# Optimization experiments

Measured on AMD Instinct MI355X. Metric: run time of the kernel, lower is better.

The kernel has to match this reference:

```python
import jax, jax.numpy as jnp
import numpy as np

D_MODEL = 1024
RANK = 256
INIT_ALPHA = 0.5


def setup_inputs() -> dict:
    key = jax.random.key(0)
    ks = jax.random.split(key, 12)
    D, R = D_MODEL, RANK
    s = 0.02
    return {
        "x": jax.random.normal(ks[0], (4, 2048, D), dtype=jnp.float32),
        "Wq": jax.random.normal(ks[1], (D, D), dtype=jnp.float32) * s,
        "Wk": jax.random.normal(ks[2], (D, D), dtype=jnp.float32) * s,
        "Wo": jax.random.normal(ks[3], (D, D), dtype=jnp.float32) * s,
        "U_b": jax.random.normal(ks[4], (D, R), dtype=jnp.float32) * s,
        "V_b": jax.random.normal(ks[5], (D, R), dtype=jnp.float32) * s,
        "W_b": jax.random.normal(ks[6], (D, R), dtype=jnp.float32) * s,
        "bias_b": jnp.zeros((D,), dtype=jnp.float32),
        "U_t": jax.random.normal(ks[7], (D, R), dtype=jnp.float32) * s,
        "V_t": jax.random.normal(ks[8], (D, R), dtype=jnp.float32) * s,
        "W_t": jax.random.normal(ks[9], (D, R), dtype=jnp.float32) * s,
        "X_t": jax.random.normal(ks[10], (D, R), dtype=jnp.float32) * s,
        "bias_t": jnp.zeros((D,), dtype=jnp.float32),
        "alpha": jnp.asarray(INIT_ALPHA, dtype=jnp.float32),
    }


def reference(x, Wq, Wk, Wo, U_b, V_b, W_b, bias_b, U_t, V_t, W_t, X_t, bias_t, alpha):
    # Math identical to the original O(T^2 D) materialization (attention_mask=None path),
    # reduced to causal cumulative sums: sum_{j<=i} (q_i * k_j) = q_i * cumsum_j(k_j).
    B, T, D = x.shape
    Q = x @ Wq.T                      # [B,T,D] (nn.Linear: x @ W^T)
    K = x @ Wk.T
    counts = jnp.arange(1, T + 1, dtype=x.dtype)[None, :, None]  # [1,T,1]
    Z = jnp.cumsum(x, axis=1) / counts  # causal cumulative mean [B,T,D]

    # Bilinear: sum_{j<=i} ((Q_i V_b) * (K_j W_b)) U_b^T + bias_b (per j)
    a_b = Q @ V_b                     # [B,T,R]
    c_b = jnp.cumsum(K @ W_b, axis=1) # [B,T,R] causal sum over j
    bil = (a_b * c_b) @ U_b.T         # [B,T,D]

    # Trilinear: sum_{j<=i} ((Q_i V_t) * (K_j W_t) * (Z_i X_t)) U_t^T + bias_t
    a_t = Q @ V_t
    c_t = jnp.cumsum(K @ W_t, axis=1)
    z_t = Z @ X_t
    tri = (a_t * z_t * c_t) @ U_t.T   # [B,T,D]

    # Per-i division by n_valid = i+1; the per-(i,j) biases average back to themselves.
    out = (bil + alpha * tri) / counts + (bias_b + alpha * bias_t)
    return out @ Wo.T                 # W_O (dropout=0 -> identity)
```

## Files before the change

kernel.cpp:

```cpp
#include <hip/hip_runtime.h>

#define D_MODEL 1024
#define RANK    256
#define NBATCH  4
#define TSEQ    2048
#define MROWS   (NBATCH * TSEQ)
#define NCAT    1280
#define NE      512

#define OFF_WQT   0u
#define OFF_WKT   524288u
#define OFF_WOB   1048576u
#define OFF_VCT   1572864u
#define OFF_WCT   1835008u
#define OFF_UCT   2097152u
#define OFF_B2    2359296u
#define OFF_PB    2360320u
#define OFF_GB    3015680u
#define OFF_Y     3277824u
#define OFF_SCR   13763584u
#define OFF_XB    13861888u
#define OFF_EB    OFF_XB

typedef __attribute__((ext_vector_type(8))) short bf16x8;
typedef __attribute__((ext_vector_type(4))) float f32x4;

__device__ __forceinline__ unsigned short f2bf(float f) {
  union { float f; unsigned u; } v; v.f = f;
  return (unsigned short)((v.u + 0x7fff + ((v.u >> 16) & 1)) >> 16);
}

__device__ __forceinline__ void gload16(const void* g, void* l) {
  __builtin_amdgcn_global_load_lds(
      (const __attribute__((address_space(1))) unsigned*)g,
      (__attribute__((address_space(3))) unsigned*)l, 16, 0, 0);
}

template <int EPI, int OBF>
__device__ __forceinline__ void mfma_tile(
    const short* __restrict__ A, const short* __restrict__ B, void* __restrict__ Cv,
    int K, int ldA, int ldB, int ldC, int m0, int n0,
    const float* __restrict__ bias, short* As, short* Bs) {
  const int tid = threadIdx.x;
  const int l = tid & 63;
  const int wv = tid >> 6;
  const int wm = (wv >> 1) * 64, wn = (wv & 1) * 64;

  const int sr = tid >> 2;
  const int sc = (tid & 3) * 8;
  const short* gA = A + (size_t)(m0 + sr) * ldA + sc;
  const short* gB = B + (size_t)(n0 + sr) * ldB + sc;
  short* lA = As + sr * 32 + sc;
  short* lB = Bs + sr * 32 + sc;

  const int arow = wm + (l & 15);
  const int brow = wn + (l & 15);
  const int kc = (l >> 4) * 8;

  f32x4 acc[4][4] = {};

  for (int k0 = 0; k0 < K; k0 += 32) {
    gload16(gA, lA);
    gload16(gA + (size_t)64 * ldA, lA + 64 * 32);
    gload16(gB, lB);
    gload16(gB + (size_t)64 * ldB, lB + 64 * 32);
    gA += 32; gB += 32;
    __syncthreads();

    bf16x8 af[4], bfr[4];
#pragma unroll
    for (int m = 0; m < 4; ++m) af[m] = *(const bf16x8*)&As[(arow + m * 16) * 32 + kc];
#pragma unroll
    for (int n = 0; n < 4; ++n) bfr[n] = *(const bf16x8*)&Bs[(brow + n * 16) * 32 + kc];

#pragma unroll
    for (int m = 0; m < 4; ++m)
#pragma unroll
      for (int n = 0; n < 4; ++n)
        acc[m][n] = __builtin_amdgcn_mfma_f32_16x16x32_bf16(af[m], bfr[n], acc[m][n], 0, 0, 0);
    __syncthreads();
  }

  const int cc = wn + (l & 15);
  const int crb = wm + (l >> 4) * 4;
#pragma unroll
  for (int m = 0; m < 4; ++m) {
#pragma unroll
    for (int j = 0; j < 4; ++j) {
      const int gm = m0 + crb + m * 16 + j;
      float inv = 1.0f;
      if (EPI) inv = 1.0f / (float)((gm & (TSEQ - 1)) + 1);
#pragma unroll
      for (int n = 0; n < 4; ++n) {
        const int gn = n0 + cc + n * 16;
        float v = acc[m][n][j];
        if (EPI) v = v * inv + bias[gn];
        if (OBF) ((short*)Cv)[(size_t)gm * ldC + gn] = (short)f2bf(v);
        else     ((float*)Cv)[(size_t)gm * ldC + gn] = v;
      }
    }
  }
}

template <int EPI>
__global__ __launch_bounds__(256) void mfma_nt(
    const short* __restrict__ A, const short* __restrict__ B,
    float* __restrict__ C, int K, int ldA, int ldB, int ldC,
    const float* __restrict__ bias) {
  __shared__ short As[128 * 32];
  __shared__ short Bs[128 * 32];
  mfma_tile<EPI, 0>(A, B, C, K, ldA, ldB, ldC,
                    blockIdx.y * 128, blockIdx.x * 128, bias, As, Bs);
}

__global__ __launch_bounds__(256) void prep_mfma(
    const short* __restrict__ VCT, const short* __restrict__ WQT,
    const short* __restrict__ WCT, const short* __restrict__ WKT,
    const short* __restrict__ WOB, const short* __restrict__ UCT,
    short* __restrict__ Pb, short* __restrict__ Gb) {
  __shared__ short As[128 * 32];
  __shared__ short Bs[128 * 32];
  const int g = blockIdx.x >> 5, t = blockIdx.x & 31;
  if (g == 0)
    mfma_tile<0, 1>(VCT, WQT, Pb, 1024, 1024, 1024, 1024,
                    (t >> 3) * 128, (t & 7) * 128, nullptr, As, Bs);
  else if (g == 1)
    mfma_tile<0, 1>(WCT, WKT, Pb + (size_t)512 * 1024, 1024, 1024, 1024, 1024,
                    (t >> 3) * 128, (t & 7) * 128, nullptr, As, Bs);
  else
    mfma_tile<0, 1>(WOB, UCT, Gb, 1024, 1024, 1024, 512,
                    (t >> 2) * 128, (t & 3) * 128, nullptr, As, Bs);
}

__global__ __launch_bounds__(256) void trans_kernel(
    const float* __restrict__ Vb, const float* __restrict__ Vt,
    const float* __restrict__ Wb, const float* __restrict__ Wt,
    const float* __restrict__ Ub, const float* __restrict__ Ut,
    const float* __restrict__ Xt, const float* __restrict__ Wq,
    const float* __restrict__ Wk,
    short* __restrict__ VCT, short* __restrict__ WCT, short* __restrict__ UCT,
    short* __restrict__ PbXt, short* __restrict__ WQT, short* __restrict__ WKT) {
  const int bid = blockIdx.x;
  const int tid = threadIdx.x;
  const float* src; short* O; int r0, d0, c0, ldS;
  if (bid < 384) {
    const int z = bid >> 7, t = bid & 127;
    r0 = (t >> 4) * 64; d0 = (t & 15) * 64; ldS = 256;
    const float* S0 = z == 0 ? Vb : z == 1 ? Wb : Ub;
    const float* S1 = z == 0 ? Vt : z == 1 ? Wt : Ut;
    O = z == 0 ? VCT : z == 1 ? WCT : UCT;
    src = (r0 < 256) ? S0 : S1; c0 = r0 & 255;
  } else if (bid < 448) {
    const int t = bid - 384;
    r0 = (t >> 4) * 64; d0 = (t & 15) * 64; ldS = 256;
    src = Xt; c0 = r0; O = PbXt;
  } else {
    const int t = bid - 448;
    const int w = t >> 8, tt = t & 255;
    r0 = (tt >> 4) * 64; d0 = (tt & 15) * 64; ldS = 1024;
    src = w ? Wk : Wq; O = w ? WKT : WQT; c0 = r0;
  }
  __shared__ float Ts[64][65];
  const int lr = tid >> 4;
  const int lc = (tid & 15) * 4;
#pragma unroll
  for (int p = 0; p < 4; ++p) {
    const int row = lr + p * 16;
    const float4 v = *(const float4*)&src[(size_t)(d0 + row) * ldS + c0 + lc];
    Ts[row][lc + 0] = v.x; Ts[row][lc + 1] = v.y;
    Ts[row][lc + 2] = v.z; Ts[row][lc + 3] = v.w;
  }
  __syncthreads();
#pragma unroll
  for (int p = 0; p < 4; ++p) {
    const int ri = lr + p * 16;
    ushort4 o;
    o.x = f2bf(Ts[lc + 0][ri]); o.y = f2bf(Ts[lc + 1][ri]);
    o.z = f2bf(Ts[lc + 2][ri]); o.w = f2bf(Ts[lc + 3][ri]);
    *(ushort4*)&((unsigned short*)O)[(size_t)(r0 + ri) * 1024 + d0 + lc] = o;
  }
}

__global__ void f2b_kernel(const float* __restrict__ in, short* __restrict__ out, int n) {
  const int i = (blockIdx.x * blockDim.x + threadIdx.x) * 4;
  if (i >= n) return;
  const float4 v = *(const float4*)&in[i];
  ushort4 o;
  o.x = f2bf(v.x); o.y = f2bf(v.y); o.z = f2bf(v.z); o.w = f2bf(v.w);
  *(ushort4*)&out[i] = o;
}

__global__ void bias_proj(const float* __restrict__ Wo, const float* __restrict__ bias_b,
                          const float* __restrict__ bias_t, const float* __restrict__ alpha_p,
                          float* __restrict__ b2) {
  const float al = *alpha_p;
  const int d = blockIdx.x;
  const int t = threadIdx.x;
  float s = 0.f;
  for (int e = t; e < 1024; e += 256)
    s += Wo[(size_t)d * 1024 + e] * (bias_b[e] + al * bias_t[e]);
  __shared__ float red[256];
  red[t] = s; __syncthreads();
  for (int off = 128; off > 0; off >>= 1) {
    if (t < off) red[t] += red[t + off];
    __syncthreads();
  }
  if (t == 0) b2[d] = red[0];
}

#define CUMCOLS 768
__global__ void cumsum_s1(const float* __restrict__ Y, float* __restrict__ scr) {
  const int lane = threadIdx.x;
  const int cg = blockIdx.x, seg = blockIdx.y, b = blockIdx.z;
  const int col = 512 + cg * 64 + lane;
  size_t base = (size_t)(b * TSEQ + seg * 64) * NCAT + col;
  float s = 0.f;
  for (int t = 0; t < 64; ++t) s += Y[base + (size_t)t * NCAT];
  scr[(size_t)(b * 32 + seg) * CUMCOLS + cg * 64 + lane] = s;
}
__global__ void cumsum_s2(float* __restrict__ scr) {
  const int lane = threadIdx.x;
  const int cg = blockIdx.x, b = blockIdx.z;
  const int c = cg * 64 + lane;
  float run = 0.f;
  for (int seg = 0; seg < 32; ++seg) {
    const size_t idx = (size_t)(b * 32 + seg) * CUMCOLS + c;
    const float v = scr[idx];
    scr[idx] = run;
    run += v;
  }
}
__global__ void cumsum_s3(float* __restrict__ Y, const float* __restrict__ scr) {
  const int lane = threadIdx.x;
  const int cg = blockIdx.x, seg = blockIdx.y, b = blockIdx.z;
  const int col = 512 + cg * 64 + lane;
  size_t base = (size_t)(b * TSEQ + seg * 64) * NCAT + col;
  float run = scr[(size_t)(b * 32 + seg) * CUMCOLS + cg * 64 + lane];
  for (int t = 0; t < 64; ++t) {
    const size_t idx = base + (size_t)t * NCAT;
    run += Y[idx];
    float o = run;
    if (col >= 1024) o *= 1.0f / (float)(seg * 64 + t + 1);
    Y[idx] = o;
  }
}

__global__ void combine_E(const float* __restrict__ Y, short* __restrict__ Eb,
                          const float* __restrict__ alpha_p) {
  const float al = *alpha_p;
  const int idx = blockIdx.x * blockDim.x + threadIdx.x;
  const int row = idx >> 9, r = idx & 511;
  const size_t rb = (size_t)row * NCAT;
  float v;
  if (r < 256) {
    v = Y[rb + r] * Y[rb + 512 + r];
  } else {
    const int r2 = r - 256;
    v = al * Y[rb + r] * Y[rb + 768 + r2] * Y[rb + 1024 + r2];
  }
  Eb[(size_t)row * 512 + r] = (short)f2bf(v);
}

extern "C" void kernel_launch(void* const* d_in, const int* in_sizes, int n_in,
                              void* d_out, int out_size, void* d_ws, size_t ws_size,
                              hipStream_t stream) {
  const float* x      = (const float*)d_in[0];
  const float* Wq     = (const float*)d_in[1];
  const float* Wk     = (const float*)d_in[2];
  const float* Wo     = (const float*)d_in[3];
  const float* Ub     = (const float*)d_in[4];
  const float* Vb     = (const float*)d_in[5];
  const float* Wb     = (const float*)d_in[6];
  const float* bias_b = (const float*)d_in[7];
  const float* Ut     = (const float*)d_in[8];
  const float* Vt     = (const float*)d_in[9];
  const float* Wt     = (const float*)d_in[10];
  const float* Xt     = (const float*)d_in[11];
  const float* bias_t = (const float*)d_in[12];
  const float* alpha  = (const float*)d_in[13];
  float* out = (float*)d_out;
  float* ws  = (float*)d_ws;

  short* WQT = (short*)(ws + OFF_WQT);
  short* WKT = (short*)(ws + OFF_WKT);
  short* WOB = (short*)(ws + OFF_WOB);
  short* VCT = (short*)(ws + OFF_VCT);
  short* WCT = (short*)(ws + OFF_WCT);
  short* UCT = (short*)(ws + OFF_UCT);
  float* b2  = ws + OFF_B2;
  short* Pb  = (short*)(ws + OFF_PB);
  short* Gb  = (short*)(ws + OFF_GB);
  float* Y   = ws + OFF_Y;
  float* scr = ws + OFF_SCR;
  short* xb  = (short*)(ws + OFF_XB);
  short* Eb  = (short*)(ws + OFF_EB);

  trans_kernel<<<960, 256, 0, stream>>>(Vb, Vt, Wb, Wt, Ub, Ut, Xt, Wq, Wk,
                                        VCT, WCT, UCT, Pb + (size_t)1024 * 1024,
                                        WQT, WKT);
  f2b_kernel<<<1024, 256, 0, stream>>>(Wo, WOB, 1024 * 1024);
  prep_mfma<<<96, 256, 0, stream>>>(VCT, WQT, WCT, WKT, WOB, UCT, Pb, Gb);
  bias_proj<<<1024, 256, 0, stream>>>(Wo, bias_b, bias_t, alpha, b2);
  f2b_kernel<<<8192, 256, 0, stream>>>(x, xb, MROWS * 1024);
  mfma_nt<0><<<dim3(NCAT / 128, MROWS / 128), 256, 0, stream>>>(
      xb, Pb, Y, 1024, 1024, 1024, NCAT, nullptr);
  cumsum_s1<<<dim3(12, 32, NBATCH), 64, 0, stream>>>(Y, scr);
  cumsum_s2<<<dim3(12, 1, NBATCH), 64, 0, stream>>>(scr);
  cumsum_s3<<<dim3(12, 32, NBATCH), 64, 0, stream>>>(Y, scr);
  combine_E<<<(MROWS * NE + 255) / 256, 256, 0, stream>>>(Y, Eb, alpha);
  mfma_nt<1><<<dim3(1024 / 128, MROWS / 128), 256, 0, stream>>>(
      Eb, Gb, out, 512, 512, 512, 1024, b2);
}
```

Before: 240.2 us.

## Double-buffer GEMM, fuse segment sums into epilogue, merge scan and combine

The MFMA tile loop now double-buffers its LDS tiles, so the global loads for the next K-step are issued before the current MFMAs run, with explicit waitcnt and barriers around them. The first GEMM's epilogue writes per-64-row segment column sums to scratch, which removes the separate cumsum_s1 pass over Y. The cumsum_s3 and combine_E kernels are merged into one scan_combine kernel that computes running sums and writes the bf16 E directly, avoiding a read-modify-write of Y. The weight and x fp32-to-bf16 conversions are folded into the transpose kernel to cut launches. The cost is doubled LDS per block, and scan_combine launches only 512 small single-wave blocks that loop serially over 64 rows, which may limit parallelism.

```diff
diff --git a/kernel.cpp b/kernel.cpp
--- a/kernel.cpp
+++ b/kernel.cpp
@@ -1,10 +1,8 @@
 #include <hip/hip_runtime.h>
 
-#define D_MODEL 1024
-#define RANK    256
 #define NBATCH  4
 #define TSEQ    2048
-#define MROWS   (NBATCH * TSEQ)
+#define MROWS   8192
 #define NCAT    1280
 #define NE      512
 
@@ -36,49 +34,77 @@
       (__attribute__((address_space(3))) unsigned*)l, 16, 0, 0);
 }
 
-template <int EPI, int OBF>
+template <int EPI, int OBF, int CS>
 __device__ __forceinline__ void mfma_tile(
     const short* __restrict__ A, const short* __restrict__ B, void* __restrict__ Cv,
     int K, int ldA, int ldB, int ldC, int m0, int n0,
-    const float* __restrict__ bias, short* As, short* Bs) {
+    const float* __restrict__ bias, float* __restrict__ scr, short* L) {
+  short* As0 = L;          short* Bs0 = L + 4096;
+  short* As1 = L + 8192;   short* Bs1 = L + 12288;
   const int tid = threadIdx.x;
   const int l = tid & 63;
   const int wv = tid >> 6;
   const int wm = (wv >> 1) * 64, wn = (wv & 1) * 64;
-
-  const int sr = tid >> 2;
-  const int sc = (tid & 3) * 8;
+  const int sr = tid >> 2, sc = (tid & 3) * 8;
   const short* gA = A + (size_t)(m0 + sr) * ldA + sc;
   const short* gB = B + (size_t)(n0 + sr) * ldB + sc;
-  short* lA = As + sr * 32 + sc;
-  short* lB = Bs + sr * 32 + sc;
-
-  const int arow = wm + (l & 15);
-  const int brow = wn + (l & 15);
+  const int so = sr * 32 + sc;
+  const int arow = wm + (l & 15), brow = wn + (l & 15);
   const int kc = (l >> 4) * 8;
 
   f32x4 acc[4][4] = {};
 
-  for (int k0 = 0; k0 < K; k0 += 32) {
-    gload16(gA, lA);
-    gload16(gA + (size_t)64 * ldA, lA + 64 * 32);
-    gload16(gB, lB);
-    gload16(gB + (size_t)64 * ldB, lB + 64 * 32);
-    gA += 32; gB += 32;
-    __syncthreads();
-
-    bf16x8 af[4], bfr[4];
-#pragma unroll
-    for (int m = 0; m < 4; ++m) af[m] = *(const bf16x8*)&As[(arow + m * 16) * 32 + kc];
-#pragma unroll
-    for (int n = 0; n < 4; ++n) bfr[n] = *(const bf16x8*)&Bs[(brow + n * 16) * 32 + kc];
-
-#pragma unroll
-    for (int m = 0; m < 4; ++m)
-#pragma unroll
-      for (int n = 0; n < 4; ++n)
-        acc[m][n] = __builtin_amdgcn_mfma_f32_16x16x32_bf16(af[m], bfr[n], acc[m][n], 0, 0, 0);
-    __syncthreads();
+  gload16(gA, As0 + so); gload16(gA + (size_t)64 * ldA, As0 + so + 2048);
+  gload16(gB, Bs0 + so); gload16(gB + (size_t)64 * ldB, Bs0 + so + 2048);
+  gA += 32; gB += 32;
+  asm volatile("s_waitcnt vmcnt(0)" ::: "memory");
+  __builtin_amdgcn_s_barrier();
+  __builtin_amdgcn_sched_barrier(0);
+
+  const int nt = K >> 5;
+  for (int t = 0; t < nt; t += 2) {
+    {
+      gload16(gA, As1 + so); gload16(gA + (size_t)64 * ldA, As1 + so + 2048);
+      gload16(gB, Bs1 + so); gload16(gB + (size_t)64 * ldB, Bs1 + so + 2048);
+      gA += 32; gB += 32;
+      bf16x8 af[4], bfr[4];
+#pragma unroll
+      for (int m = 0; m < 4; ++m) af[m] = *(const bf16x8*)&As0[(arow + m * 16) * 32 + kc];
+#pragma unroll
+      for (int n = 0; n < 4; ++n) bfr[n] = *(const bf16x8*)&Bs0[(brow + n * 16) * 32 + kc];
+      asm volatile("s_waitcnt lgkmcnt(0)" ::: "memory");
+      __builtin_amdgcn_sched_barrier(0);
+#pragma unroll
+      for (int m = 0; m < 4; ++m)
+#pragma unroll
+        for (int n = 0; n < 4; ++n)
+          acc[m][n] = __builtin_amdgcn_mfma_f32_16x16x32_bf16(af[m], bfr[n], acc[m][n], 0, 0, 0);
+      asm volatile("s_waitcnt vmcnt(0)" ::: "memory");
+      __builtin_amdgcn_s_barrier();
+      __builtin_amdgcn_sched_barrier(0);
+    }
+    {
+      if (t + 2 < nt) {
+        gload16(gA, As0 + so); gload16(gA + (size_t)64 * ldA, As0 + so + 2048);
+        gload16(gB, Bs0 + so); gload16(gB + (size_t)64 * ldB, Bs0 + so + 2048);
+        gA += 32; gB += 32;
+      }
+      bf16x8 af[4], bfr[4];
+#pragma unroll
+      for (int m = 0; m < 4; ++m) af[m] = *(const bf16x8*)&As1[(arow + m * 16) * 32 + kc];
+#pragma unroll
+      for (int n = 0; n < 4; ++n) bfr[n] = *(const bf16x8*)&Bs1[(brow + n * 16) * 32 + kc];
+      asm volatile("s_waitcnt lgkmcnt(0)" ::: "memory");
+      __builtin_amdgcn_sched_barrier(0);
+#pragma unroll
+      for (int m = 0; m < 4; ++m)
+#pragma unroll
+        for (int n = 0; n < 4; ++n)
+          acc[m][n] = __builtin_amdgcn_mfma_f32_16x16x32_bf16(af[m], bfr[n], acc[m][n], 0, 0, 0);
+      asm volatile("s_waitcnt vmcnt(0)" ::: "memory");
+      __builtin_amdgcn_s_barrier();
+      __builtin_amdgcn_sched_barrier(0);
+    }
   }
 
   const int cc = wn + (l & 15);
@@ -100,17 +126,32 @@
       }
     }
   }
-}
-
-template <int EPI>
+  if (CS && n0 >= 512) {
+    const int bb = (m0 + wm) >> 11;
+    const int seg = ((m0 + wm) & (TSEQ - 1)) >> 6;
+    float* sp = scr + (size_t)(bb * 32 + seg) * 768 + (n0 - 512);
+#pragma unroll
+    for (int n = 0; n < 4; ++n) {
+      float s = 0.f;
+#pragma unroll
+      for (int m = 0; m < 4; ++m)
+#pragma unroll
+        for (int j = 0; j < 4; ++j) s += acc[m][n][j];
+      s += __shfl_xor(s, 16, 64);
+      s += __shfl_xor(s, 32, 64);
+      if (l < 16) sp[cc + n * 16] = s;
+    }
+  }
+}
+
+template <int EPI, int CS>
 __global__ __launch_bounds__(256) void mfma_nt(
     const short* __restrict__ A, const short* __restrict__ B,
     float* __restrict__ C, int K, int ldA, int ldB, int ldC,
-    const float* __restrict__ bias) {
-  __shared__ short As[128 * 32];
-  __shared__ short Bs[128 * 32];
-  mfma_tile<EPI, 0>(A, B, C, K, ldA, ldB, ldC,
-                    blockIdx.y * 128, blockIdx.x * 128, bias, As, Bs);
+    const float* __restrict__ bias, float* __restrict__ scr) {
+  __shared__ short L[16384];
+  mfma_tile<EPI, 0, CS>(A, B, C, K, ldA, ldB, ldC,
+                        blockIdx.y * 128, blockIdx.x * 128, bias, scr, L);
 }
 
 __global__ __launch_bounds__(256) void prep_mfma(
@@ -118,30 +159,42 @@
     const short* __restrict__ WCT, const short* __restrict__ WKT,
     const short* __restrict__ WOB, const short* __restrict__ UCT,
     short* __restrict__ Pb, short* __restrict__ Gb) {
-  __shared__ short As[128 * 32];
-  __shared__ short Bs[128 * 32];
+  __shared__ short L[16384];
   const int g = blockIdx.x >> 5, t = blockIdx.x & 31;
   if (g == 0)
-    mfma_tile<0, 1>(VCT, WQT, Pb, 1024, 1024, 1024, 1024,
-                    (t >> 3) * 128, (t & 7) * 128, nullptr, As, Bs);
+    mfma_tile<0, 1, 0>(VCT, WQT, Pb, 1024, 1024, 1024, 1024,
+                       (t >> 3) * 128, (t & 7) * 128, nullptr, nullptr, L);
   else if (g == 1)
-    mfma_tile<0, 1>(WCT, WKT, Pb + (size_t)512 * 1024, 1024, 1024, 1024, 1024,
-                    (t >> 3) * 128, (t & 7) * 128, nullptr, As, Bs);
+    mfma_tile<0, 1, 0>(WCT, WKT, Pb + (size_t)512 * 1024, 1024, 1024, 1024, 1024,
+                       (t >> 3) * 128, (t & 7) * 128, nullptr, nullptr, L);
   else
-    mfma_tile<0, 1>(WOB, UCT, Gb, 1024, 1024, 1024, 512,
-                    (t >> 2) * 128, (t & 3) * 128, nullptr, As, Bs);
-}
-
-__global__ __launch_bounds__(256) void trans_kernel(
+    mfma_tile<0, 1, 0>(WOB, UCT, Gb, 1024, 1024, 1024, 512,
+                       (t >> 2) * 128, (t & 3) * 128, nullptr, nullptr, L);
+}
+
+__global__ __launch_bounds__(256) void prep_all(
     const float* __restrict__ Vb, const float* __restrict__ Vt,
     const float* __restrict__ Wb, const float* __restrict__ Wt,
     const float* __restrict__ Ub, const float* __restrict__ Ut,
     const float* __restrict__ Xt, const float* __restrict__ Wq,
-    const float* __restrict__ Wk,
+    const float* __restrict__ Wk, const float* __restrict__ Wo,
+    const float* __restrict__ x,
     short* __restrict__ VCT, short* __restrict__ WCT, short* __restrict__ UCT,
-    short* __restrict__ PbXt, short* __restrict__ WQT, short* __restrict__ WKT) {
+    short* __restrict__ PbXt, short* __restrict__ WQT, short* __restrict__ WKT,
+    short* __restrict__ WOB, short* __restrict__ xb) {
   const int bid = blockIdx.x;
   const int tid = threadIdx.x;
+  if (bid >= 960) {
+    const size_t j = ((size_t)(bid - 960) * 256 + tid) * 4;
+    const int isWo = j < 1048576u;
+    const float* s = isWo ? &Wo[j] : &x[j - 1048576u];
+    const float4 v = *(const float4*)s;
+    ushort4 o;
+    o.x = f2bf(v.x); o.y = f2bf(v.y); o.z = f2bf(v.z); o.w = f2bf(v.w);
+    unsigned short* dst = (unsigned short*)(isWo ? WOB : xb);
+    *(ushort4*)&dst[isWo ? j : j - 1048576u] = o;
+    return;
+  }
   const float* src; short* O; int r0, d0, c0, ldS;
   if (bid < 384) {
     const int z = bid >> 7, t = bid & 127;
@@ -181,15 +234,6 @@
   }
 }
 
-__global__ void f2b_kernel(const float* __restrict__ in, short* __restrict__ out, int n) {
-  const int i = (blockIdx.x * blockDim.x + threadIdx.x) * 4;
-  if (i >= n) return;
-  const float4 v = *(const float4*)&in[i];
-  ushort4 o;
-  o.x = f2bf(v.x); o.y = f2bf(v.y); o.z = f2bf(v.z); o.w = f2bf(v.w);
-  *(ushort4*)&out[i] = o;
-}
-
 __global__ void bias_proj(const float* __restrict__ Wo, const float* __restrict__ bias_b,
                           const float* __restrict__ bias_t, const float* __restrict__ alpha_p,
                           float* __restrict__ b2) {
@@ -208,57 +252,49 @@
   if (t == 0) b2[d] = red[0];
 }
 
-#define CUMCOLS 768
-__global__ void cumsum_s1(const float* __restrict__ Y, float* __restrict__ scr) {
-  const int lane = threadIdx.x;
-  const int cg = blockIdx.x, seg = blockIdx.y, b = blockIdx.z;
-  const int col = 512 + cg * 64 + lane;
-  size_t base = (size_t)(b * TSEQ + seg * 64) * NCAT + col;
-  float s = 0.f;
-  for (int t = 0; t < 64; ++t) s += Y[base + (size_t)t * NCAT];
-  scr[(size_t)(b * 32 + seg) * CUMCOLS + cg * 64 + lane] = s;
-}
 __global__ void cumsum_s2(float* __restrict__ scr) {
   const int lane = threadIdx.x;
   const int cg = blockIdx.x, b = blockIdx.z;
   const int c = cg * 64 + lane;
   float run = 0.f;
   for (int seg = 0; seg < 32; ++seg) {
-    const size_t idx = (size_t)(b * 32 + seg) * CUMCOLS + c;
+    const size_t idx = (size_t)(b * 32 + seg) * 768 + c;
     const float v = scr[idx];
     scr[idx] = run;
     run += v;
   }
 }
-__global__ void cumsum_s3(float* __restrict__ Y, const float* __restrict__ scr) {
+
+__global__ __launch_bounds__(64) void scan_combine(
+    const float* __restrict__ Y, const float* __restrict__ scr,
+    short* __restrict__ Eb, const float* __restrict__ alpha_p) {
+  const float al = *alpha_p;
   const int lane = threadIdx.x;
-  const int cg = blockIdx.x, seg = blockIdx.y, b = blockIdx.z;
-  const int col = 512 + cg * 64 + lane;
-  size_t base = (size_t)(b * TSEQ + seg * 64) * NCAT + col;
-  float run = scr[(size_t)(b * 32 + seg) * CUMCOLS + cg * 64 + lane];
-  for (int t = 0; t < 64; ++t) {
-    const size_t idx = base + (size_t)t * NCAT;
-    run += Y[idx];
-    float o = run;
-    if (col >= 1024) o *= 1.0f / (float)(seg * 64 + t + 1);
-    Y[idx] = o;
-  }
-}
-
-__global__ void combine_E(const float* __restrict__ Y, short* __restrict__ Eb,
-                          const float* __restrict__ alpha_p) {
-  const float al = *alpha_p;
-  const int idx = blockIdx.x * blockDim.x + threadIdx.x;
-  const int row = idx >> 9, r = idx & 511;
-  const size_t rb = (size_t)row * NCAT;
-  float v;
-  if (r < 256) {
-    v = Y[rb + r] * Y[rb + 512 + r];
-  } else {
-    const int r2 = r - 256;
-    v = al * Y[rb + r] * Y[rb + 768 + r2] * Y[rb + 1024 + r2];
-  }
-  Eb[(size_t)row * 512 + r] = (short)f2bf(v);
+  const int g = blockIdx.x, seg = blockIdx.y, b = blockIdx.z;
+  const int c2 = g * 64 + lane;
+  const float* sc = scr + (size_t)(b * 32 + seg) * 768;
+  float run_cb = sc[c2];
+  float run_ct = sc[256 + c2];
+  float run_zt = sc[512 + c2];
+  const size_t row0 = (size_t)(b * TSEQ + seg * 64);
+  const float* yr = Y + row0 * NCAT;
+  float ab = yr[c2], at = yr[256 + c2];
+  float cb = yr[512 + c2], ct = yr[768 + c2], zt = yr[1024 + c2];
+  for (int tt = 0; tt < 64; ++tt) {
+    float nab = 0, nat = 0, ncb = 0, nct = 0, nzt = 0;
+    if (tt < 63) {
+      const float* yn = yr + NCAT;
+      nab = yn[c2]; nat = yn[256 + c2];
+      ncb = yn[512 + c2]; nct = yn[768 + c2]; nzt = yn[1024 + c2];
+    }
+    run_cb += cb; run_ct += ct; run_zt += zt;
+    const float inv = 1.0f / (float)(seg * 64 + tt + 1);
+    short* er = Eb + (row0 + tt) * 512;
+    er[c2]       = (short)f2bf(ab * run_cb);
+    er[256 + c2] = (short)f2bf(al * at * (run_zt * inv) * run_ct);
+    ab = nab; at = nat; cb = ncb; ct = nct; zt = nzt;
+    yr += NCAT;
+  }
 }
 
 extern "C" void kernel_launch(void* const* d_in, const int* in_sizes, int n_in,
@@ -295,19 +331,15 @@
   short* xb  = (short*)(ws + OFF_XB);
   short* Eb  = (short*)(ws + OFF_EB);
 
-  trans_kernel<<<960, 256, 0, stream>>>(Vb, Vt, Wb, Wt, Ub, Ut, Xt, Wq, Wk,
-                                        VCT, WCT, UCT, Pb + (size_t)1024 * 1024,
-                                        WQT, WKT);
-  f2b_kernel<<<1024, 256, 0, stream>>>(Wo, WOB, 1024 * 1024);
+  prep_all<<<10176, 256, 0, stream>>>(Vb, Vt, Wb, Wt, Ub, Ut, Xt, Wq, Wk, Wo, x,
+                                      VCT, WCT, UCT, Pb + (size_t)1024 * 1024,
+                                      WQT, WKT, WOB, xb);
   prep_mfma<<<96, 256, 0, stream>>>(VCT, WQT, WCT, WKT, WOB, UCT, Pb, Gb);
   bias_proj<<<1024, 256, 0, stream>>>(Wo, bias_b, bias_t, alpha, b2);
-  f2b_kernel<<<8192, 256, 0, stream>>>(x, xb, MROWS * 1024);
-  mfma_nt<0><<<dim3(NCAT / 128, MROWS / 128), 256, 0, stream>>>(
-      xb, Pb, Y, 1024, 1024, 1024, NCAT, nullptr);
-  cumsum_s1<<<dim3(12, 32, NBATCH), 64, 0, stream>>>(Y, scr);
+  mfma_nt<0, 1><<<dim3(NCAT / 128, MROWS / 128), 256, 0, stream>>>(
+      xb, Pb, Y, 1024, 1024, 1024, NCAT, nullptr, scr);
   cumsum_s2<<<dim3(12, 1, NBATCH), 64, 0, stream>>>(scr);
-  cumsum_s3<<<dim3(12, 32, NBATCH), 64, 0, stream>>>(Y, scr);
-  combine_E<<<(MROWS * NE + 255) / 256, 256, 0, stream>>>(Y, Eb, alpha);
-  mfma_nt<1><<<dim3(1024 / 128, MROWS / 128), 256, 0, stream>>>(
-      Eb, Gb, out, 512, 512, 512, 1024, b2);
-}
+  scan_combine<<<dim3(4, 32, NBATCH), 64, 0, stream>>>(Y, scr, Eb, alpha);
+  mfma_nt<1, 0><<<dim3(1024 / 128, MROWS / 128), 256, 0, stream>>>(
+      Eb, Gb, out, 512, 512, 512, 1024, b2, nullptr);
+}
```

After: 228.0 us. -5.0%, faster.
